# Kernel tuning notes

Measured on AMD Instinct MI355X. Metric: run time of the kernel, lower is better.

The kernel has to match this reference:

```python
import jax, jax.numpy as jnp
import numpy as np

T, B, H = 512, 256, 512

def setup_inputs() -> dict:
    key = jax.random.key(0)
    k1, k2, k3, k4 = jax.random.split(key, 4)
    inputs = jax.random.normal(k1, (T, B, H), jnp.float32)
    resets = jax.random.randint(k2, (T, B), 0, 2).astype(bool)
    # flax OptimizedLSTMCell params: fused 4H gate projections (gate order i, f, g, o)
    scale = 1.0 / np.sqrt(H).astype(np.float32)
    Wi = jax.random.normal(k3, (H, 4 * H), jnp.float32) * scale  # input kernel (no bias)
    Wh = jax.random.normal(k4, (H, 4 * H), jnp.float32) * scale  # hidden kernel
    b = jnp.zeros((4 * H,), jnp.float32)                         # hidden bias
    c0 = jnp.zeros((B, H), jnp.float32)
    h0 = jnp.zeros((B, H), jnp.float32)
    return {"inputs": inputs, "resets": resets, "c0": c0, "h0": h0,
            "Wi": Wi, "Wh": Wh, "b": b}

def reference(inputs, resets, c0, h0, Wi, Wh, b):
    # inputs: [T, B, H], resets: [T, B] bool. initialize_carry is zeros, so
    # the reset masking zeroes (c, h) where resets is True before the cell step.
    def step(carry, xt):
        c, h = carry
        x, r = xt
        m = r[:, None]
        c = jnp.where(m, 0.0, c)
        h = jnp.where(m, 0.0, h)
        gates = x @ Wi + h @ Wh + b           # [B, 4H]
        i, f, g, o = jnp.split(gates, 4, axis=-1)
        c_new = jax.nn.sigmoid(f) * c + jax.nn.sigmoid(i) * jnp.tanh(g)
        h_new = jax.nn.sigmoid(o) * jnp.tanh(c_new)
        return (c_new, h_new), h_new
    (c_f, h_f), ys = jax.lax.scan(step, (c0, h0), (inputs, resets))
    return ys, c_f, h_f
```

## Files before the change

### kernel.cpp

```cpp
#include <hip/hip_runtime.h>

#define TT 512
#define BB 256
#define HH 512
#define FH 2048

typedef __attribute__((ext_vector_type(8))) short short8;
typedef __attribute__((ext_vector_type(4))) short short4v;
typedef __attribute__((ext_vector_type(4))) float f32x4;
typedef __attribute__((ext_vector_type(2))) float f32x2;

__device__ __forceinline__ short f2bf(float f) {
  union { float f; unsigned u; } v; v.f = f;
  unsigned r = v.u + 0x7fffu + ((v.u >> 16) & 1u);
  return (short)(r >> 16);
}
__device__ __forceinline__ unsigned short f2h(float f) {
  union { _Float16 h; unsigned short u; } v;
  v.h = (_Float16)f;
  return v.u;
}
__device__ __forceinline__ float h2f(unsigned short u) {
  union { _Float16 h; unsigned short u; } v;
  v.u = u;
  return (float)v.h;
}

__device__ __forceinline__ float sigm(float x) {
  return 1.f / (1.f + __expf(-x));
}
__device__ __forceinline__ float tanh_fast(float x) {
  float e = __expf(2.f * x);
  return 1.f - 2.f / (e + 1.f);
}

__device__ __forceinline__ void gload16(const void* g, void* l) {
  __builtin_amdgcn_global_load_lds(
      (const __attribute__((address_space(1))) unsigned*)g,
      (__attribute__((address_space(3))) unsigned*)(unsigned)(unsigned long long)l,
      16, 0, 0);
}

__global__ void prep_kernel(const float* __restrict__ Wi, const float* __restrict__ Wh,
                            const float* __restrict__ h0, const float* __restrict__ c0,
                            const float* __restrict__ x,
                            short* __restrict__ WiT, short* __restrict__ WhT,
                            unsigned* __restrict__ hb0, float* __restrict__ cb,
                            short* __restrict__ hbf, short* __restrict__ Xb,
                            int* __restrict__ done) {
  int idx = blockIdx.x * blockDim.x + threadIdx.x;
  int stride = gridDim.x * blockDim.x;
  for (int i = idx; i < FH * HH; i += stride) {
    int col = i >> 9;
    int k = i & 511;
    WiT[i] = f2bf(Wi[(size_t)k * FH + col]);
    WhT[i] = f2bf(Wh[(size_t)k * FH + col]);
  }
  for (int i = idx; i < BB * HH; i += stride) {
    hbf[i] = f2bf(h0[i]);
    cb[i] = c0[i];
  }
  for (int i = idx; i < BB * 256; i += stride) {
    int row = i >> 8;
    int cpx = (i & 255) * 2;
    hb0[i] = (unsigned)(unsigned short)f2bf(h0[(size_t)row * HH + cpx]) |
             ((unsigned)(unsigned short)f2bf(h0[(size_t)row * HH + cpx + 1]) << 16);
  }
  for (int i = idx; i < 8 * TT * 32; i += stride) done[i] = 0;
  const size_t nx4 = (size_t)TT * BB * HH / 4;
  for (size_t i = idx; i < nx4; i += stride) {
    f32x4 v = *(const f32x4*)(x + i * 4);
    short4v s = { f2bf(v[0]), f2bf(v[1]), f2bf(v[2]), f2bf(v[3]) };
    *(short4v*)(Xb + i * 4) = s;
  }
}

__global__ __launch_bounds__(256) void precomp_kernel(
    const short* __restrict__ Xb, const short* __restrict__ WiT,
    const float* __restrict__ bias, unsigned short* __restrict__ Gx,
    int rowBase) {
  __shared__ short As[128 * 64];
  __shared__ short Bs[128 * 64];

  const int tid = threadIdx.x;
  const int cb0 = blockIdx.x * 128;
  const int rb = blockIdx.y * 128;
  const size_t grow = (size_t)rowBase + rb;

  const int wid = tid >> 6;
  const int lane = tid & 63;
  const int lc = lane & 15;
  const int kg = lane >> 4;
  const int m0 = (wid >> 1) * 64;
  const int n0 = (wid & 1) * 64;

  const int srow0 = wid * 32;
  const int lrow = lane >> 3;
  const int lkc = lane & 7;

  f32x4 acc[4][4] = {};

  for (int kt = 0; kt < 8; ++kt) {
    const int k0 = kt * 64;
    __syncthreads();
#pragma unroll
    for (int i = 0; i < 4; ++i) {
      const int row = srow0 + i * 8 + lrow;
      gload16(Xb + (grow + row) * 512 + k0 + lkc * 8,
              (char*)As + (size_t)(srow0 + i * 8) * 128);
      gload16(WiT + (size_t)(cb0 + row) * 512 + k0 + lkc * 8,
              (char*)Bs + (size_t)(srow0 + i * 8) * 128);
    }
    __syncthreads();

#pragma unroll
    for (int ks = 0; ks < 2; ++ks) {
      const int kb = ks * 64 + kg * 16;
      short8 af[4], bf[4];
#pragma unroll
      for (int m = 0; m < 4; ++m)
        af[m] = *(const short8*)((char*)As + (m0 + m * 16 + lc) * 128 + kb);
#pragma unroll
      for (int n = 0; n < 4; ++n)
        bf[n] = *(const short8*)((char*)Bs + (n0 + n * 16 + lc) * 128 + kb);
#pragma unroll
      for (int m = 0; m < 4; ++m)
#pragma unroll
        for (int n = 0; n < 4; ++n)
          acc[m][n] = __builtin_amdgcn_mfma_f32_16x16x32_bf16(af[m], bf[n],
                                                              acc[m][n], 0, 0, 0);
    }
  }

#pragma unroll
  for (int n = 0; n < 4; ++n) {
    const int col = cb0 + n0 + n * 16 + lc;
    const float bv = bias[col];
#pragma unroll
    for (int m = 0; m < 4; ++m) {
      const int rloc = rb + m0 + m * 16 + kg * 4;
#pragma unroll
      for (int j = 0; j < 4; ++j)
        Gx[(size_t)(rloc + j) * FH + col] = f2h(acc[m][n][j] + bv);
    }
  }
}

__global__ __launch_bounds__(256) void lstm_persist(
    const int* __restrict__ resets,
    const short* __restrict__ WhT,
    const unsigned short* __restrict__ Gx,
    unsigned* __restrict__ hbA,
    unsigned* __restrict__ hbB,
    float* __restrict__ cb,
    float* __restrict__ out,
    int* __restrict__ done,
    int t0, int ct) {
  extern __shared__ short whs[];
  __shared__ short ah[32 * 512];
  __shared__ float gex[4 * 32 * 17];

  const int tid = threadIdx.x;
  const int bid = blockIdx.x;
  const int grp = bid >> 5;
  const int j = bid & 31;
  const int rb = grp * 32;
  const int hc0 = j * 16;

  const int wid = tid >> 6;
  const int lane = tid & 63;
  const int lc = lane & 15;
  const int kg = lane >> 4;

  {
    const int lcol = tid >> 2;
    const int part = tid & 3;
    const int g = lcol >> 4;
    const int gcol = g * 512 + hc0 + (lcol & 15);
    const short* src = WhT + (size_t)gcol * 512 + part * 128;
    const int dbase = lcol * 1024 + part * 256;
    const int sw = (lcol & 7) << 4;
#pragma unroll
    for (int it = 0; it < 16; ++it) {
      short8 v = *(const short8*)(src + it * 8);
      *(short8*)((char*)whs + ((dbase + it * 16) ^ sw)) = v;
    }
  }

  const int erow = tid >> 3;
  const int cp = (tid & 7) * 2;
  float creg[2];
  {
    const float* cs = cb + (size_t)(rb + erow) * HH + hc0 + cp;
    creg[0] = cs[0];
    creg[1] = cs[1];
  }

  __syncthreads();

  for (int t = t0; t < t0 + ct; ++t) {
    const unsigned short* gxb =
        Gx + ((size_t)(t - t0) * BB + (rb + erow)) * FH + hc0 + cp;
    unsigned gxu[4];
#pragma unroll
    for (int g = 0; g < 4; ++g) gxu[g] = *(const unsigned*)(gxb + g * 512);
    const int* rstT = resets + (size_t)t * BB;
    const int rstE = rstT[rb + erow];

    if (t > t0) {
      if (wid == 0) {
        int* dn = done + ((size_t)grp * TT + (t - 1)) * 32;
        bool ok;
        do {
          int v = (lane < 32)
                      ? __hip_atomic_load(&dn[lane], __ATOMIC_RELAXED,
                                          __HIP_MEMORY_SCOPE_AGENT)
                      : 1;
          ok = __all(v != 0);
          if (!ok) __builtin_amdgcn_s_sleep(2);
        } while (!ok);
      }
      __syncthreads();
    }

    {
      unsigned* hsrc = ((t & 1) ? hbB : hbA) + (size_t)rb * 256;
      unsigned hv[32];
#pragma unroll
      for (int it = 0; it < 32; ++it)
        hv[it] = __hip_atomic_load(&hsrc[it * 256 + tid], __ATOMIC_RELAXED,
                                   __HIP_MEMORY_SCOPE_AGENT);
#pragma unroll
      for (int it = 0; it < 32; ++it) {
        unsigned v = (rstT[rb + it] != 0) ? 0u : hv[it];
        *(unsigned*)((char*)ah + ((it * 1024 + tid * 4) ^ ((it & 7) << 4))) = v;
      }
    }
    __syncthreads();

    {
      const int sw = (lc & 7) << 4;
      f32x4 acc[2] = {};
#pragma unroll
      for (int kk = 0; kk < 16; ++kk) {
        const int kb = kk * 64 + kg * 16;
        short8 a0 = *(const short8*)((char*)ah + ((lc * 1024 + kb) ^ sw));
        short8 a1 = *(const short8*)((char*)ah + (((lc + 16) * 1024 + kb) ^ sw));
        short8 b = *(const short8*)((char*)whs +
                      (((wid * 16 + lc) * 1024 + kb) ^ sw));
        acc[0] = __builtin_amdgcn_mfma_f32_16x16x32_bf16(a0, b, acc[0], 0, 0, 0);
        acc[1] = __builtin_amdgcn_mfma_f32_16x16x32_bf16(a1, b, acc[1], 0, 0, 0);
      }
#pragma unroll
      for (int m = 0; m < 2; ++m)
#pragma unroll
        for (int jj = 0; jj < 4; ++jj)
          gex[wid * 544 + (m * 16 + kg * 4 + jj) * 17 + lc] = acc[m][jj];
    }
    __syncthreads();

    {
      unsigned* hdst = (t & 1) ? hbA : hbB;
      const int gb = erow * 17 + cp;
      float gi0 = gex[0 * 544 + gb] + h2f((unsigned short)(gxu[0] & 0xffffu));
      float gi1 = gex[0 * 544 + gb + 1] + h2f((unsigned short)(gxu[0] >> 16));
      float gf0 = gex[1 * 544 + gb] + h2f((unsigned short)(gxu[1] & 0xffffu));
      float gf1 = gex[1 * 544 + gb + 1] + h2f((unsigned short)(gxu[1] >> 16));
      float gg0 = gex[2 * 544 + gb] + h2f((unsigned short)(gxu[2] & 0xffffu));
      float gg1 = gex[2 * 544 + gb + 1] + h2f((unsigned short)(gxu[2] >> 16));
      float go0 = gex[3 * 544 + gb] + h2f((unsigned short)(gxu[3] & 0xffffu));
      float go1 = gex[3 * 544 + gb + 1] + h2f((unsigned short)(gxu[3] >> 16));
      float cold0 = rstE ? 0.f : creg[0];
      float cold1 = rstE ? 0.f : creg[1];
      float cn0 = sigm(gf0) * cold0 + sigm(gi0) * tanh_fast(gg0);
      float cn1 = sigm(gf1) * cold1 + sigm(gi1) * tanh_fast(gg1);
      float hn0 = sigm(go0) * tanh_fast(cn0);
      float hn1 = sigm(go1) * tanh_fast(cn1);
      creg[0] = cn0;
      creg[1] = cn1;
      unsigned pack = (unsigned)(unsigned short)f2bf(hn0) |
                      ((unsigned)(unsigned short)f2bf(hn1) << 16);
      __hip_atomic_store(&hdst[(size_t)(rb + erow) * 256 + (hc0 >> 1) + (tid & 7)],
                         pack, __ATOMIC_RELAXED, __HIP_MEMORY_SCOPE_AGENT);
      asm volatile("s_waitcnt vmcnt(0)" ::: "memory");
      __syncthreads();
      if (tid == 0)
        __hip_atomic_store(&done[((size_t)grp * TT + t) * 32 + j], 1,
                           __ATOMIC_RELAXED, __HIP_MEMORY_SCOPE_AGENT);
      size_t gidx = (size_t)(rb + erow) * HH + hc0 + cp;
      *(f32x2*)(out + (size_t)t * BB * HH + gidx) = (f32x2){hn0, hn1};
      if (t == TT - 1) {
        out[(size_t)TT * BB * HH + gidx] = cn0;
        out[(size_t)TT * BB * HH + gidx + 1] = cn1;
        out[(size_t)TT * BB * HH + (size_t)BB * HH + gidx] = hn0;
        out[(size_t)TT * BB * HH + (size_t)BB * HH + gidx + 1] = hn1;
      }
    }
  }

  {
    float* cs = cb + (size_t)(rb + erow) * HH + hc0 + cp;
    cs[0] = creg[0];
    cs[1] = creg[1];
  }
}

__global__ __launch_bounds__(64) void lstm_step_fullk(
    const float* __restrict__ xt, const int* __restrict__ rst,
    const float* __restrict__ bias, const short* __restrict__ WiT,
    const short* __restrict__ WhT, const short* __restrict__ hin,
    short* __restrict__ hout, float* __restrict__ cbuf, float* __restrict__ ys) {
  const int lane = threadIdx.x;
  const int lc = lane & 15;
  const int kg = lane >> 4;
  const int r0 = blockIdx.x * 16;
  const int h0 = blockIdx.y * 16;
  const int hc = h0 + lc;

  float coldv[4];
  int rstj[4];
#pragma unroll
  for (int jj = 0; jj < 4; ++jj) {
    int row = r0 + kg * 4 + jj;
    rstj[jj] = rst[row];
    coldv[jj] = cbuf[(size_t)row * HH + hc];
  }

  const int rowA = r0 + lc;
  const bool rm = rst[rowA] != 0;
  const short8 zero = {};
  f32x4 acc[4] = {};
#pragma unroll
  for (int kk = 0; kk < 16; ++kk) {
    const int ko = kk * 32 + kg * 8;
    f32x4 u0 = *(const f32x4*)(xt + (size_t)rowA * HH + ko);
    f32x4 u1 = *(const f32x4*)(xt + (size_t)rowA * HH + ko + 4);
    short8 a;
#pragma unroll
    for (int e = 0; e < 4; ++e) { a[e] = f2bf(u0[e]); a[e + 4] = f2bf(u1[e]); }
#pragma unroll
    for (int g = 0; g < 4; ++g) {
      const short8 b = *(const short8*)(WiT + (size_t)(g * HH + h0 + lc) * HH + ko);
      acc[g] = __builtin_amdgcn_mfma_f32_16x16x32_bf16(a, b, acc[g], 0, 0, 0);
    }
  }
#pragma unroll
  for (int kk = 0; kk < 16; ++kk) {
    const int ko = kk * 32 + kg * 8;
    short8 a = rm ? zero : *(const short8*)(hin + (size_t)rowA * HH + ko);
#pragma unroll
    for (int g = 0; g < 4; ++g) {
      const short8 b = *(const short8*)(WhT + (size_t)(g * HH + h0 + lc) * HH + ko);
      acc[g] = __builtin_amdgcn_mfma_f32_16x16x32_bf16(a, b, acc[g], 0, 0, 0);
    }
  }

#pragma unroll
  for (int jj = 0; jj < 4; ++jj) {
    int row = r0 + kg * 4 + jj;
    float gi = acc[0][jj] + bias[0 * HH + hc];
    float gf = acc[1][jj] + bias[1 * HH + hc];
    float gg = acc[2][jj] + bias[2 * HH + hc];
    float go = acc[3][jj] + bias[3 * HH + hc];
    float cold = rstj[jj] ? 0.f : coldv[jj];
    float cn = sigm(gf) * cold + sigm(gi) * tanh_fast(gg);
    float hn = sigm(go) * tanh_fast(cn);
    cbuf[(size_t)row * HH + hc] = cn;
    hout[(size_t)row * HH + hc] = f2bf(hn);
    ys[(size_t)row * HH + hc] = hn;
  }
}

__global__ void finalize_kernel(const float* __restrict__ cbuf, float* __restrict__ out) {
  int i = blockIdx.x * blockDim.x + threadIdx.x;
  if (i < BB * HH) {
    size_t base = (size_t)TT * BB * HH;
    out[base + i] = cbuf[i];
    out[base + BB * HH + i] = out[(size_t)(TT - 1) * BB * HH + i];
  }
}

extern "C" void kernel_launch(void* const* d_in, const int* in_sizes, int n_in,
                              void* d_out, int out_size, void* d_ws, size_t ws_size,
                              hipStream_t stream) {
  const float* x      = (const float*)d_in[0];
  const int*   resets = (const int*)d_in[1];
  const float* c0     = (const float*)d_in[2];
  const float* h0     = (const float*)d_in[3];
  const float* Wi     = (const float*)d_in[4];
  const float* Wh     = (const float*)d_in[5];
  const float* bias   = (const float*)d_in[6];
  float* out = (float*)d_out;

  char* ws = (char*)d_ws;
  short* WiT = (short*)ws;
  short* WhT = (short*)(ws + (2u << 20));
  unsigned* hb0 = (unsigned*)(ws + (4u << 20));
  unsigned* hb1 = (unsigned*)(ws + (4u << 20) + (256u << 10));
  float* cb  = (float*)(ws + (4u << 20) + (512u << 10));
  short* hbf0 = (short*)(ws + (5u << 20));
  short* hbf1 = hbf0 + BB * HH;
  int*   dn  = (int*)(ws + (5u << 20) + (512u << 10));
  short* Xb  = (short*)(ws + (6u << 20));
  const size_t GX_OFF = (6u << 20) + (size_t)TT * BB * HH * 2;
  unsigned short* Gx = (unsigned short*)(ws + GX_OFF);

  const size_t perT = (size_t)BB * FH * 2;
  int chunkT = 0;
  if (ws_size > GX_OFF + perT) chunkT = (int)((ws_size - GX_OFF) / perT);
  if (chunkT > TT) chunkT = TT;
  chunkT &= ~1;

  prep_kernel<<<2048, 256, 0, stream>>>(Wi, Wh, h0, c0, x, WiT, WhT,
                                        hb0, cb, hbf0, Xb, dn);

  if (chunkT >= 2) {
    for (int t0 = 0; t0 < TT; t0 += chunkT) {
      int ct = (TT - t0 < chunkT) ? (TT - t0) : chunkT;
      precomp_kernel<<<dim3(16, ct * 2), 256, 0, stream>>>(Xb, WiT, bias, Gx, t0 * BB);
      lstm_persist<<<256, 256, 65536, stream>>>(resets, WhT, Gx, hb0, hb1,
                                                cb, out, dn, t0, ct);
    }
  } else {
    for (int t = 0; t < TT; ++t) {
      const short* hin = (t & 1) ? hbf1 : hbf0;
      short* hout      = (t & 1) ? hbf0 : hbf1;
      lstm_step_fullk<<<dim3(16, 32), 64, 0, stream>>>(
          x + (size_t)t * BB * HH, resets + (size_t)t * BB, bias, WiT, WhT,
          hin, hout, cb, out + (size_t)t * BB * HH);
    }
    finalize_kernel<<<(BB * HH + 255) / 256, 256, 0, stream>>>(cb, out);
  }
}
```

Before: 2.413 ms.

## Tile the weight transpose through LDS and remap precompute GEMM blocks across XCDs

Weight transpose and bf16 conversion move into their own kernel that stages 64x64 tiles in shared memory. Global reads and writes become coalesced, replacing the strided per-element gather in the old prep loop. The input-projection GEMM now runs on a 1D grid, with block IDs mapped so that consecutive blocks on the same XCD share row tiles, aiming for better L2 reuse of Xb. Chunk length is rounded to a multiple of 4 so the grid size is divisible by 128, which the swizzle requires.

Result: no change. 2.390 ms (-1.0%).

```diff
diff --git a/kernel.cpp b/kernel.cpp
--- a/kernel.cpp
+++ b/kernel.cpp
@@ -41,21 +41,52 @@
       16, 0, 0);
 }
 
-__global__ void prep_kernel(const float* __restrict__ Wi, const float* __restrict__ Wh,
-                            const float* __restrict__ h0, const float* __restrict__ c0,
+__global__ __launch_bounds__(256) void prep_w(
+    const float* __restrict__ Wi, const float* __restrict__ Wh,
+    short* __restrict__ WiT, short* __restrict__ WhT) {
+  __shared__ short t[64][65];
+  const int w = blockIdx.x >> 8;
+  const int tile = blockIdx.x & 255;
+  const int c0 = (tile & 31) * 64;
+  const int k0 = (tile >> 5) * 64;
+  const float* src = w ? Wh : Wi;
+  short* dst = w ? WhT : WiT;
+  const int tid = threadIdx.x;
+
+  {
+    const int r = tid >> 2;
+    const int cq = (tid & 3) * 16;
+#pragma unroll
+    for (int i = 0; i < 4; ++i) {
+      f32x4 v = *(const f32x4*)(src + (size_t)(k0 + r) * FH + c0 + cq + i * 4);
+      short4v s = { f2bf(v[0]), f2bf(v[1]), f2bf(v[2]), f2bf(v[3]) };
+      *(short4v*)(&t[r][cq + i * 4]) = s;
+    }
+  }
+  __syncthreads();
+
+  {
+    const int c = tid >> 2;
+    const int kq = (tid & 3) * 16;
+    short8 o0, o1;
+#pragma unroll
+    for (int e = 0; e < 8; ++e) {
+      o0[e] = t[kq + e][c];
+      o1[e] = t[kq + 8 + e][c];
+    }
+    short* d = dst + (size_t)(c0 + c) * 512 + k0 + kq;
+    *(short8*)d = o0;
+    *(short8*)(d + 8) = o1;
+  }
+}
+
+__global__ void prep_kernel(const float* __restrict__ h0, const float* __restrict__ c0,
                             const float* __restrict__ x,
-                            short* __restrict__ WiT, short* __restrict__ WhT,
                             unsigned* __restrict__ hb0, float* __restrict__ cb,
                             short* __restrict__ hbf, short* __restrict__ Xb,
                             int* __restrict__ done) {
   int idx = blockIdx.x * blockDim.x + threadIdx.x;
   int stride = gridDim.x * blockDim.x;
-  for (int i = idx; i < FH * HH; i += stride) {
-    int col = i >> 9;
-    int k = i & 511;
-    WiT[i] = f2bf(Wi[(size_t)k * FH + col]);
-    WhT[i] = f2bf(Wh[(size_t)k * FH + col]);
-  }
   for (int i = idx; i < BB * HH; i += stride) {
     hbf[i] = f2bf(h0[i]);
     cb[i] = c0[i];
@@ -83,8 +114,20 @@
   __shared__ short Bs[128 * 64];
 
   const int tid = threadIdx.x;
-  const int cb0 = blockIdx.x * 128;
-  const int rb = blockIdx.y * 128;
+
+  int coltile, rowtile;
+  if ((gridDim.x & 127) == 0) {
+    const int b = blockIdx.x;
+    const int xcd = b & 7;
+    const int i = b >> 3;
+    rowtile = (i >> 4) * 8 + xcd;
+    coltile = i & 15;
+  } else {
+    coltile = blockIdx.x & 15;
+    rowtile = blockIdx.x >> 4;
+  }
+  const int cb0 = coltile * 128;
+  const int rb = rowtile * 128;
   const size_t grow = (size_t)rowBase + rb;
 
   const int wid = tid >> 6;
@@ -409,15 +452,15 @@
   int chunkT = 0;
   if (ws_size > GX_OFF + perT) chunkT = (int)((ws_size - GX_OFF) / perT);
   if (chunkT > TT) chunkT = TT;
-  chunkT &= ~1;
-
-  prep_kernel<<<2048, 256, 0, stream>>>(Wi, Wh, h0, c0, x, WiT, WhT,
-                                        hb0, cb, hbf0, Xb, dn);
-
-  if (chunkT >= 2) {
+  chunkT &= ~3;
+
+  prep_w<<<512, 256, 0, stream>>>(Wi, Wh, WiT, WhT);
+  prep_kernel<<<2048, 256, 0, stream>>>(h0, c0, x, hb0, cb, hbf0, Xb, dn);
+
+  if (chunkT >= 4) {
     for (int t0 = 0; t0 < TT; t0 += chunkT) {
       int ct = (TT - t0 < chunkT) ? (TT - t0) : chunkT;
-      precomp_kernel<<<dim3(16, ct * 2), 256, 0, stream>>>(Xb, WiT, bias, Gx, t0 * BB);
+      precomp_kernel<<<ct * 32, 256, 0, stream>>>(Xb, WiT, bias, Gx, t0 * BB);
       lstm_persist<<<256, 256, 65536, stream>>>(resets, WhT, Gx, hb0, hb1,
                                                 cb, out, dn, t0, ct);
     }
```
